# Kernel optimization log

Hardware: AMD Instinct MI355X
Metric: run time of the kernel (lower is better)

The kernel has to match this reference:

```python
import jax, jax.numpy as jnp
import numpy as np

B, G, H, K = 2, 16, 128, 8      # batch, grid side, hidden, edges per grid point
TG = B * G ** 3                  # total grid points = 8192
E = TG * K                       # total edges = 65536
N = 2048                         # total atoms
EPS = 1e-5


def _bn(x, g, b):
    # eval-mode BatchNorm3d with running_mean=0, running_var=1
    s = g / jnp.sqrt(1.0 + EPS)
    return x * s[None, :, None, None, None] + b[None, :, None, None, None]


def _conv(x, w, pad):
    return jax.lax.conv_general_dilated(
        x, w, window_strides=(1, 1, 1), padding=[(pad, pad)] * 3,
        dimension_numbers=("NCDHW", "OIDHW", "NCDHW"))


def _mlp2(x, w1, b1, w2, b2, act):
    return act(x @ w1 + b1) @ w2 + b2


def setup_inputs() -> dict:
    key = jax.random.key(0)
    ks = jax.random.split(key, 16)
    def nrm(k, shape, scale=1.0):
        return jax.random.normal(k, shape, dtype=jnp.float32) * scale
    def lin(k, i, o):
        return nrm(k, (i, o), 1.0 / np.sqrt(i))
    return {
        "node_embedding": nrm(ks[0], (N, H)),
        "node_pos": nrm(ks[1], (N, 3)),
        "grid_pos": nrm(ks[2], (TG, 3)),
        "edge_row": jax.random.randint(ks[3], (E,), 0, N),
        # every grid point covered K times -> bincount never zero (matches original's div-by-bincount)
        "edge_col": jnp.repeat(jnp.arange(TG), K),
        "edge_w1": lin(ks[4], 6, H),    "edge_b1": jnp.zeros(H),
        "edge_w2": lin(ks[5], H, H),    "edge_b2": jnp.zeros(H),
        "msg_w1": lin(ks[6], 2 * H, H), "msg_b1": jnp.zeros(H),
        "msg_w2": lin(ks[7], H, H),     "msg_b2": jnp.zeros(H),
        "upd_w1": lin(ks[8], H, H),     "upd_b1": jnp.zeros(H),
        "upd_w2": lin(ks[9], H, H),     "upd_b2": jnp.zeros(H),
        "in_gamma": jnp.ones(H), "in_beta": jnp.zeros(H),
        "blk_conv1": nrm(ks[10], (3, H, H, 3, 3, 3), 1.0 / np.sqrt(H * 27)),
        "blk_bn1_g": jnp.ones((3, H)), "blk_bn1_b": jnp.zeros((3, H)),
        "blk_conv2": nrm(ks[11], (3, H, H, 3, 3, 3), 1.0 / np.sqrt(H * 27)),
        "blk_bn2_g": jnp.ones((3, H)), "blk_bn2_b": jnp.zeros((3, H)),
        "blk_conv5": nrm(ks[12], (3, H, H, 5, 5, 5), 1.0 / np.sqrt(H * 125)),
        "blk_bns_g": jnp.ones((3, H)), "blk_bns_b": jnp.zeros((3, H)),
        "fc_w": lin(ks[13], H, 20), "fc_b": jnp.zeros(20),
    }


def reference(node_embedding, node_pos, grid_pos, edge_row, edge_col,
              edge_w1, edge_b1, edge_w2, edge_b2,
              msg_w1, msg_b1, msg_w2, msg_b2,
              upd_w1, upd_b1, upd_w2, upd_b2,
              in_gamma, in_beta,
              blk_conv1, blk_bn1_g, blk_bn1_b,
              blk_conv2, blk_bn2_g, blk_bn2_b,
              blk_conv5, blk_bns_g, blk_bns_b,
              fc_w, fc_b):
    silu = jax.nn.silu
    # ---- MPNN message: gather -> edge MLP -> message MLP ----
    edge_attr = jnp.concatenate([node_pos[edge_row], grid_pos[edge_col]], axis=-1)  # [E,6]
    pos_emb = _mlp2(edge_attr, edge_w1, edge_b1, edge_w2, edge_b2, silu)            # [E,H]
    msg_in = jnp.concatenate([node_embedding[edge_row], pos_emb], axis=-1)          # [E,2H]
    message = _mlp2(msg_in, msg_w1, msg_b1, msg_w2, msg_b2, silu)                   # [E,H]
    # ---- scatter-mean onto grid points (global_add_pool / bincount) ----
    agg = jax.ops.segment_sum(message, edge_col, num_segments=TG)
    cnt = jax.ops.segment_sum(jnp.ones((E,), jnp.float32), edge_col, num_segments=TG)
    agg = agg / cnt[:, None]
    x = _mlp2(agg, upd_w1, upd_b1, upd_w2, upd_b2, silu)                            # [TG,H]
    # ---- to dense grid, channels-first ----
    x = x.reshape(B, G, G, G, H).transpose(0, 4, 1, 2, 3)                           # [B,H,G,G,G]
    x = _bn(x, in_gamma, in_beta)
    # ---- 3 residual blocks (eval BN, dropout identity) ----
    for i in range(3):
        left = jax.nn.relu(_bn(_conv(x, blk_conv1[i], 1), blk_bn1_g[i], blk_bn1_b[i]))
        left = _bn(_conv(left, blk_conv2[i], 1), blk_bn2_g[i], blk_bn2_b[i])
        short = _bn(_conv(x, blk_conv5[i], 2), blk_bns_g[i], blk_bns_b[i])
        x = jax.nn.relu(left + short)
    # ---- global max pool (kernel == spatial size) + fc + log_softmax ----
    pooled = x.max(axis=(2, 3, 4))                                                  # [B,H]
    logits = pooled @ fc_w + fc_b                                                   # [B,20]
    return jax.nn.log_softmax(logits, axis=-1)
```

## Files before the change

### kernel.cpp

```cpp
#include <hip/hip_runtime.h>
#include <math.h>


#define EPS_BN 1e-5f

typedef _Float16 f16x8 __attribute__((ext_vector_type(8)));
typedef float f32x4 __attribute__((ext_vector_type(4)));

struct us4 { unsigned short x, y, z, w; };

__device__ __forceinline__ float silu_f(float x) {
  return x / (1.0f + __expf(-x));
}
__device__ __forceinline__ unsigned short f2h(float x) {
  union { _Float16 h; unsigned short u; } v; v.h = (_Float16)x; return v.u;
}
__device__ __forceinline__ float h2f(unsigned short u) {
  union { unsigned short u; _Float16 h; } v; v.u = u; return (float)v.h;
}

template<int AMODE, int KTOT>
__global__ __launch_bounds__(256, 2)
void gemm_k(const float* __restrict__ A,
            const float* __restrict__ W,
            const float* __restrict__ bias,
            const float* __restrict__ pscale,
            const float* __restrict__ pshift,
            float* __restrict__ C,
            int act, int obf)
{
  __shared__ __align__(16) float As[32][68];
  __shared__ __align__(16) float Bs[32][128];
  const int t = threadIdx.x;
  const int mbase = blockIdx.x * 64;
  const int m0 = (t >> 4) << 2;
  const int nA = (t & 15) << 2;
  const int ml = t >> 2;
  const int ks = (t & 3) << 3;

  float acc[4][8];
#pragma unroll
  for (int i = 0; i < 4; i++)
#pragma unroll
    for (int j = 0; j < 8; j++) acc[i][j] = 0.f;

  for (int k0 = 0; k0 < KTOT; k0 += 32) {
    {
      const float* src = A + (size_t)(mbase + ml) * KTOT + (k0 + ks);
      const float4 a0 = *(const float4*)src;
      const float4 a1 = *(const float4*)(src + 4);
      As[ks+0][ml]=a0.x; As[ks+1][ml]=a0.y; As[ks+2][ml]=a0.z; As[ks+3][ml]=a0.w;
      As[ks+4][ml]=a1.x; As[ks+5][ml]=a1.y; As[ks+6][ml]=a1.z; As[ks+7][ml]=a1.w;
    }
    {
      const int kl = t >> 3;
      const int ns = (t & 7) << 4;
      const float* wsrc = W + (size_t)(k0 + kl) * 128 + ns;
      *(float4*)&Bs[kl][ns +  0] = *(const float4*)(wsrc + 0);
      *(float4*)&Bs[kl][ns +  4] = *(const float4*)(wsrc + 4);
      *(float4*)&Bs[kl][ns +  8] = *(const float4*)(wsrc + 8);
      *(float4*)&Bs[kl][ns + 12] = *(const float4*)(wsrc + 12);
    }
    __syncthreads();
#pragma unroll 8
    for (int kk = 0; kk < 32; kk++) {
      const float4 av = *(const float4*)&As[kk][m0];
      const float4 b0 = *(const float4*)&Bs[kk][nA];
      const float4 b1 = *(const float4*)&Bs[kk][nA + 64];
      const float a[4]  = {av.x, av.y, av.z, av.w};
      const float bb[8] = {b0.x, b0.y, b0.z, b0.w, b1.x, b1.y, b1.z, b1.w};
#pragma unroll
      for (int i = 0; i < 4; i++)
#pragma unroll
        for (int j = 0; j < 8; j++)
          acc[i][j] = fmaf(a[i], bb[j], acc[i][j]);
    }
    __syncthreads();
  }

  const float rs = rsqrtf(1.f + EPS_BN);
#pragma unroll
  for (int i = 0; i < 4; i++) {
    const size_t row = (size_t)(mbase + m0 + i);
    float v[8];
#pragma unroll
    for (int j = 0; j < 8; j++) {
      const int col = (j < 4) ? (nA + j) : (nA + 60 + j);
      float x = acc[i][j] + bias[col];
      if (act == 1) x = silu_f(x);
      if (pscale) x = fmaf(x, pscale[col] * rs, pshift[col]);
      v[j] = x;
    }
    if (obf) {
      unsigned short* Cb = (unsigned short*)C;
      us4 r0, r1;
      r0.x=f2h(v[0]); r0.y=f2h(v[1]); r0.z=f2h(v[2]); r0.w=f2h(v[3]);
      r1.x=f2h(v[4]); r1.y=f2h(v[5]); r1.z=f2h(v[6]); r1.w=f2h(v[7]);
      *(us4*)&Cb[row * 128 + nA]      = r0;
      *(us4*)&Cb[row * 128 + nA + 64] = r1;
    } else {
      *(float4*)&C[row * 128 + nA]      = make_float4(v[0], v[1], v[2], v[3]);
      *(float4*)&C[row * 128 + nA + 64] = make_float4(v[4], v[5], v[6], v[7]);
    }
  }
}

__global__ __launch_bounds__(256)
void wpack_g_k(const float* __restrict__ w, unsigned short* __restrict__ wp,
               int total)
{
  const int i = blockIdx.x * 256 + threadIdx.x;
  if (i >= total) return;
  const int j   = i & 7;
  const int l   = (i >> 3) & 63;
  const int nt  = (i >> 9) & 7;
  const int kq  = (i >> 12) & 3;
  const int tap = i >> 14;
  const int k = tap * 128 + kq * 32 + (l >> 4) * 8 + j;
  const int n = nt * 16 + (l & 15);
  wp[i] = f2h(w[(size_t)k * 128 + n]);
}

__global__ __launch_bounds__(256)
void cvt_k(const float* __restrict__ src, unsigned short* __restrict__ dst, int n)
{
  const int i = blockIdx.x * 256 + threadIdx.x;
  if (i < n) dst[i] = f2h(src[i]);
}

template<int AMODE, int TAPS>
__global__ __launch_bounds__(256)
void mgemm_k(const unsigned short* __restrict__ A,
             const unsigned short* __restrict__ emb16,
             const int* __restrict__ rows,
             const int* __restrict__ cols,
             const float* __restrict__ npos,
             const float* __restrict__ gpos,
             const float* __restrict__ ew1,
             const float* __restrict__ eb1,
             const unsigned short* __restrict__ wpanel,
             const float* __restrict__ bias,
             unsigned short* __restrict__ C,
             float* __restrict__ aggout,
             int act)
{
  __shared__ __align__(16) unsigned short Ab[64 * 128];
  __shared__ __align__(16) unsigned short Bb[16384];
  const int t = threadIdx.x;
  const int mbase = blockIdx.x * 64;
  const int l = t & 63, w = t >> 6;
  const int lx = l & 15, lq = l >> 4;
  const int mb = (w >> 1) << 1;
  const int nb = (w & 1) << 2;
  const int rowl = t >> 2;
  const int seg  = t & 3;

  float at0=0,at1=0,at2=0,at3=0,at4=0,at5=0;
  int rowm = 0;
  if (AMODE == 1) {
    const int e = mbase + rowl;
    const int r = rows[e];
    const int g = cols[e];
    at0 = npos[r*3+0]; at1 = npos[r*3+1]; at2 = npos[r*3+2];
    at3 = gpos[g*3+0]; at4 = gpos[g*3+1]; at5 = gpos[g*3+2];
  } else if (AMODE == 2) {
    rowm = rows[mbase + rowl];
  }

  f32x4 acc[2][4];
#pragma unroll
  for (int i = 0; i < 2; i++)
#pragma unroll
    for (int j = 0; j < 4; j++) acc[i][j] = (f32x4){0.f, 0.f, 0.f, 0.f};

  for (int tap = 0; tap < TAPS; tap++) {
    __syncthreads();
    if (AMODE == 1) {
#pragma unroll
      for (int uu = 0; uu < 4; uu++) {
        union { unsigned short h[8]; uint4 v; } pk;
#pragma unroll
        for (int jj = 0; jj < 8; jj++) {
          const int k = seg * 32 + uu * 8 + jj;
          float s = eb1[k];
          s = fmaf(at0, ew1[      k], s);
          s = fmaf(at1, ew1[128 + k], s);
          s = fmaf(at2, ew1[256 + k], s);
          s = fmaf(at3, ew1[384 + k], s);
          s = fmaf(at4, ew1[512 + k], s);
          s = fmaf(at5, ew1[640 + k], s);
          pk.h[jj] = f2h(silu_f(s));
        }
        const int u = seg * 4 + uu;
        *(uint4*)(Ab + (size_t)(rowl * 16 + (u ^ (rowl & 7))) * 8) = pk.v;
      }
    } else {
      const unsigned short* src;
      if (AMODE == 2) {
        src = (tap == 0) ? (emb16 + (size_t)rowm * 128 + seg * 32)
                         : (A + (size_t)(mbase + rowl) * 128 + seg * 32);
      } else {
        src = A + (size_t)(mbase + rowl) * 128 + seg * 32;
      }
#pragma unroll
      for (int uu = 0; uu < 4; uu++) {
        const uint4 v = *(const uint4*)(src + uu * 8);
        const int u = seg * 4 + uu;
        *(uint4*)(Ab + (size_t)(rowl * 16 + (u ^ (rowl & 7))) * 8) = v;
      }
    }
    {
      const unsigned short* g = wpanel + (size_t)tap * 16384 + t * 8;
      unsigned short* dl = Bb + t * 8;
#pragma unroll
      for (int r = 0; r < 8; r++) {
        __builtin_amdgcn_global_load_lds(
            (const __attribute__((address_space(1))) unsigned int*)(g + r * 2048),
            (__attribute__((address_space(3))) unsigned int*)(dl + r * 2048),
            16, 0, 0);
      }
    }
    __syncthreads();
    const int xm = lx & 7;
#pragma unroll
    for (int kq = 0; kq < 4; kq++) {
      f16x8 a0 = *(const f16x8*)(Ab + (size_t)(((mb + 0) * 16 + lx) * 16 + ((kq * 4 + lq) ^ xm)) * 8);
      f16x8 a1 = *(const f16x8*)(Ab + (size_t)(((mb + 1) * 16 + lx) * 16 + ((kq * 4 + lq) ^ xm)) * 8);
      const unsigned short* bbase = Bb + (size_t)((kq * 8 + nb) * 64 + l) * 8;
#pragma unroll
      for (int j = 0; j < 4; j++) {
        f16x8 bv = *(const f16x8*)(bbase + (size_t)j * 512);
        acc[0][j] = __builtin_amdgcn_mfma_f32_16x16x32_f16(a0, bv, acc[0][j], 0, 0, 0);
        acc[1][j] = __builtin_amdgcn_mfma_f32_16x16x32_f16(a1, bv, acc[1][j], 0, 0, 0);
      }
    }
  }

  __syncthreads();
#pragma unroll
  for (int i = 0; i < 2; i++) {
#pragma unroll
    for (int r = 0; r < 4; r++) {
      const int rowloc = (mb + i) * 16 + lq * 4 + r;
#pragma unroll
      for (int j = 0; j < 4; j++) {
        const int col = (nb + j) * 16 + lx;
        float x = acc[i][j][r] + bias[col];
        if (act == 1) x = silu_f(x);
        Ab[rowloc * 128 + col] = f2h(x);
      }
    }
  }
  __syncthreads();
  if (aggout) {
#pragma unroll
    for (int q = t * 4; q < t * 4 + 4; q++) {
      const int g = q >> 7, c = q & 127;
      float s = 0.f;
#pragma unroll
      for (int r = 0; r < 8; r++) s += h2f(Ab[(g * 8 + r) * 128 + c]);
      aggout[(size_t)((mbase >> 3) + g) * 128 + c] = s * 0.125f;
    }
  } else {
    const size_t base = (size_t)(mbase + rowl) * 128 + seg * 32;
#pragma unroll
    for (int uu = 0; uu < 4; uu++)
      *(uint4*)(C + base + uu * 8) = *(const uint4*)(Ab + rowl * 128 + seg * 32 + uu * 8);
  }
}

__global__ __launch_bounds__(256)
void wpack_k(const float* __restrict__ w, unsigned short* __restrict__ wp, int T)
{
  const int i = blockIdx.x * 256 + threadIdx.x;
  if (i >= 3 * 4 * 8 * 64 * 8) return;
  const int j  = i & 7;
  const int l  = (i >> 3) & 63;
  const int nt = (i >> 9) & 7;
  const int kq = (i >> 12) & 3;
  const int ib = i >> 14;
  const int o = nt * 16 + (l & 15);
  const int c = kq * 32 + (l >> 4) * 8 + j;
  const float* src = w + ((size_t)(ib * 128 + o) * 128 + c) * T;
  unsigned short* dst = wp + (size_t)(ib * T) * 16384
                           + (size_t)(kq * 8 + nt) * 512 + l * 8 + j;
  for (int tp = 0; tp < T; tp++)
    dst[(size_t)tp * 16384] = f2h(src[tp]);
}

template<int KS>
__global__ __launch_bounds__(256, 1)
void convmf_k(const unsigned short* __restrict__ xin,
              const unsigned short* __restrict__ wpack,
              float* __restrict__ part)
{
  constexpr int P  = KS / 2;
  constexpr int SW = 16 + 2 * P;
  __shared__ __align__(16) unsigned short Ab[4 * SW * 128];
  __shared__ __align__(16) unsigned short Bb[16384];

  const int t   = threadIdx.x;
  const int bx  = blockIdx.x;
  const int kd  = bx >> 7;
  const int rem = bx & 127;
  const int b   = rem >> 6;
  const int z   = (rem >> 2) & 15;
  const int y0  = (rem & 3) << 2;
  const int zz  = z + kd - P;
  float* pout = part + (size_t)kd * (8192 * 128);
  const size_t obase = ((size_t)((b * 16 + z) * 16 + y0) * 16) * 128;

  if ((unsigned)zz >= 16u) {
    float4 zf = make_float4(0, 0, 0, 0);
    float4* dst = (float4*)(pout + obase);
    for (int i = t; i < 2048; i += 256) dst[i] = zf;
    return;
  }

  const int l  = t & 63, w = t >> 6;
  const int lx = l & 15, lq = l >> 4;
  const int mb = (w >> 1) << 1;
  const int nb = (w & 1) << 2;

  f32x4 acc[2][4];
#pragma unroll
  for (int i = 0; i < 2; i++)
#pragma unroll
    for (int j = 0; j < 4; j++) acc[i][j] = (f32x4){0.f, 0.f, 0.f, 0.f};

  const unsigned short* inplane = xin + ((size_t)(b * 16 + zz) * 256) * 128;
  const unsigned short* wkd = wpack + (size_t)(kd * KS * KS) * 16384;

  for (int kh = 0; kh < KS; kh++) {
    __syncthreads();
    for (int idx = t; idx < 4 * SW * 16; idx += 256) {
      const int ry = idx / (SW * 16);
      const int r2 = idx - ry * (SW * 16);
      const int xs = r2 >> 4;
      const int u  = r2 & 15;
      const int y  = y0 + ry + kh - P;
      const int x  = xs - P;
      uint4 val = make_uint4(0, 0, 0, 0);
      if ((unsigned)y < 16u && (unsigned)x < 16u)
        val = *(const uint4*)(inplane + ((size_t)(y * 16 + x)) * 128 + u * 8);
      const int du = (ry * SW + xs) * 16 + (u ^ (xs & 7));
      *(uint4*)(Ab + (size_t)du * 8) = val;
    }
    const unsigned short* wkh = wkd + (size_t)(kh * KS) * 16384;
    for (int kw = 0; kw < KS; kw++) {
      __syncthreads();
      {
        const unsigned short* g = wkh + (size_t)kw * 16384 + t * 8;
        unsigned short* dl = Bb + t * 8;
#pragma unroll
        for (int r = 0; r < 8; r++) {
          __builtin_amdgcn_global_load_lds(
              (const __attribute__((address_space(1))) unsigned int*)(g + r * 2048),
              (__attribute__((address_space(3))) unsigned int*)(dl + r * 2048),
              16, 0, 0);
        }
      }
      __syncthreads();
      const int xsw = lx + kw;
      const int xm  = xsw & 7;
#pragma unroll
      for (int kq = 0; kq < 4; kq++) {
        f16x8 a0 = *(const f16x8*)(Ab + (size_t)(((mb + 0) * SW + xsw) * 16 + ((kq * 4 + lq) ^ xm)) * 8);
        f16x8 a1 = *(const f16x8*)(Ab + (size_t)(((mb + 1) * SW + xsw) * 16 + ((kq * 4 + lq) ^ xm)) * 8);
        const unsigned short* bbase = Bb + (size_t)((kq * 8 + nb) * 64 + l) * 8;
#pragma unroll
        for (int j = 0; j < 4; j++) {
          f16x8 bv = *(const f16x8*)(bbase + (size_t)j * 512);
          acc[0][j] = __builtin_amdgcn_mfma_f32_16x16x32_f16(a0, bv, acc[0][j], 0, 0, 0);
          acc[1][j] = __builtin_amdgcn_mfma_f32_16x16x32_f16(a1, bv, acc[1][j], 0, 0, 0);
        }
      }
    }
  }

#pragma unroll
  for (int i = 0; i < 2; i++) {
    const int my = mb + i;
#pragma unroll
    for (int r = 0; r < 4; r++) {
      const size_t vrow = obase + (size_t)(my * 16 + lq * 4 + r) * 128;
#pragma unroll
      for (int j = 0; j < 4; j++)
        pout[vrow + (nb + j) * 16 + lx] = acc[i][j][r];
    }
  }
}

__global__ __launch_bounds__(256)
void combine1_k(const float* __restrict__ p,
                const float* __restrict__ g, const float* __restrict__ be,
                unsigned short* __restrict__ o)
{
  const int i = blockIdx.x * 256 + threadIdx.x;
  const size_t off = (size_t)i * 4;
  const int c = (i & 31) * 4;
  float4 a0 = *(const float4*)(p + off);
  float4 a1 = *(const float4*)(p + 1048576 + off);
  float4 a2 = *(const float4*)(p + 2097152 + off);
  const float rs = rsqrtf(1.f + EPS_BN);
  float4 gg = *(const float4*)(g + c);
  float4 bb = *(const float4*)(be + c);
  float v0 = fmaxf(fmaf(a0.x + a1.x + a2.x, gg.x * rs, bb.x), 0.f);
  float v1 = fmaxf(fmaf(a0.y + a1.y + a2.y, gg.y * rs, bb.y), 0.f);
  float v2 = fmaxf(fmaf(a0.z + a1.z + a2.z, gg.z * rs, bb.z), 0.f);
  float v3 = fmaxf(fmaf(a0.w + a1.w + a2.w, gg.w * rs, bb.w), 0.f);
  us4 r; r.x = f2h(v0); r.y = f2h(v1); r.z = f2h(v2); r.w = f2h(v3);
  *(us4*)(o + off) = r;
}

__global__ __launch_bounds__(256)
void combine2_k(const float* __restrict__ p2, const float* __restrict__ p5,
                const float* __restrict__ g2, const float* __restrict__ b2,
                const float* __restrict__ gs, const float* __restrict__ bs,
                unsigned short* __restrict__ o)
{
  const int i = blockIdx.x * 256 + threadIdx.x;
  const size_t off = (size_t)i * 4;
  const int c = (i & 31) * 4;
  float4 s2 = *(const float4*)(p2 + off);
  {
    float4 a1 = *(const float4*)(p2 + 1048576 + off);
    float4 a2 = *(const float4*)(p2 + 2097152 + off);
    s2.x += a1.x + a2.x; s2.y += a1.y + a2.y;
    s2.z += a1.z + a2.z; s2.w += a1.w + a2.w;
  }
  float4 s5 = *(const float4*)(p5 + off);
#pragma unroll
  for (int gi = 1; gi < 5; gi++) {
    float4 a = *(const float4*)(p5 + (size_t)gi * 1048576 + off);
    s5.x += a.x; s5.y += a.y; s5.z += a.z; s5.w += a.w;
  }
  const float rs = rsqrtf(1.f + EPS_BN);
  float4 gg2 = *(const float4*)(g2 + c);
  float4 bb2 = *(const float4*)(b2 + c);
  float4 ggs = *(const float4*)(gs + c);
  float4 bbs = *(const float4*)(bs + c);
  float v0 = fmaxf(fmaf(s2.x, gg2.x * rs, bb2.x) + fmaf(s5.x, ggs.x * rs, bbs.x), 0.f);
  float v1 = fmaxf(fmaf(s2.y, gg2.y * rs, bb2.y) + fmaf(s5.y, ggs.y * rs, bbs.y), 0.f);
  float v2 = fmaxf(fmaf(s2.z, gg2.z * rs, bb2.z) + fmaf(s5.z, ggs.z * rs, bbs.z), 0.f);
  float v3 = fmaxf(fmaf(s2.w, gg2.w * rs, bb2.w) + fmaf(s5.w, ggs.w * rs, bbs.w), 0.f);
  us4 r; r.x = f2h(v0); r.y = f2h(v1); r.z = f2h(v2); r.w = f2h(v3);
  *(us4*)(o + off) = r;
}

__global__ __launch_bounds__(256)
void pool_partial_k(const unsigned short* __restrict__ xg, float* __restrict__ pmax)
{
  __shared__ float red[256];
  const int bz = blockIdx.x;
  const int t = threadIdx.x;
  const int c = t & 127;
  const int h = t >> 7;
  const unsigned short* base = xg + (size_t)bz * 256 * 128;
  float m = -3.4e38f;
  for (int i = 0; i < 128; i++)
    m = fmaxf(m, h2f(base[(size_t)(h * 128 + i) * 128 + c]));
  red[t] = m;
  __syncthreads();
  if (t < 128) pmax[bz * 128 + t] = fmaxf(red[t], red[t + 128]);
}

__global__ __launch_bounds__(256)
void final_k(const float* __restrict__ pmax,
             const float* __restrict__ fc_w,
             const float* __restrict__ fc_b,
             float* __restrict__ outp)
{
  __shared__ float pool[2][128];
  __shared__ float lg[2][20];
  const int t = threadIdx.x;
  const int b = t >> 7;
  const int c = t & 127;
  float m = -3.4e38f;
  for (int zi = 0; zi < 16; zi++)
    m = fmaxf(m, pmax[(b * 16 + zi) * 128 + c]);
  pool[b][c] = m;
  __syncthreads();
  if (t < 40) {
    const int bb = t / 20, j = t % 20;
    float l = fc_b[j];
    for (int cc = 0; cc < 128; cc++)
      l = fmaf(pool[bb][cc], fc_w[cc * 20 + j], l);
    lg[bb][j] = l;
  }
  __syncthreads();
  if (t < 2) {
    float mx = -3.4e38f;
    for (int j = 0; j < 20; j++) mx = fmaxf(mx, lg[t][j]);
    float s = 0.f;
    for (int j = 0; j < 20; j++) s += expf(lg[t][j] - mx);
    const float ls = mx + logf(s);
    for (int j = 0; j < 20; j++) outp[t * 20 + j] = lg[t][j] - ls;
  }
}

extern "C" void kernel_launch(void* const* d_in, const int* in_sizes, int n_in,
                              void* d_out, int out_size, void* d_ws, size_t ws_size,
                              hipStream_t stream) {
  (void)in_sizes; (void)n_in; (void)out_size; (void)ws_size;
  const float* node_embedding = (const float*)d_in[0];
  const float* node_pos  = (const float*)d_in[1];
  const float* grid_pos  = (const float*)d_in[2];
  const int*   edge_row  = (const int*)d_in[3];
  const int*   edge_col  = (const int*)d_in[4];
  const float* edge_w1   = (const float*)d_in[5];
  const float* edge_b1   = (const float*)d_in[6];
  const float* edge_w2   = (const float*)d_in[7];
  const float* edge_b2   = (const float*)d_in[8];
  const float* msg_w1    = (const float*)d_in[9];
  const float* msg_b1    = (const float*)d_in[10];
  const float* msg_w2    = (const float*)d_in[11];
  const float* msg_b2    = (const float*)d_in[12];
  const float* upd_w1    = (const float*)d_in[13];
  const float* upd_b1    = (const float*)d_in[14];
  const float* upd_w2    = (const float*)d_in[15];
  const float* upd_b2    = (const float*)d_in[16];
  const float* in_gamma  = (const float*)d_in[17];
  const float* in_beta   = (const float*)d_in[18];
  const float* blk_conv1 = (const float*)d_in[19];
  const float* blk_bn1_g = (const float*)d_in[20];
  const float* blk_bn1_b = (const float*)d_in[21];
  const float* blk_conv2 = (const float*)d_in[22];
  const float* blk_bn2_g = (const float*)d_in[23];
  const float* blk_bn2_b = (const float*)d_in[24];
  const float* blk_conv5 = (const float*)d_in[25];
  const float* blk_bns_g = (const float*)d_in[26];
  const float* blk_bns_b = (const float*)d_in[27];
  const float* fc_w      = (const float*)d_in[28];
  const float* fc_b      = (const float*)d_in[29];

  float* ws = (float*)d_ws;
  unsigned short* bufA = (unsigned short*)ws;
  unsigned short* bufB = (unsigned short*)(ws + 4194304);
  unsigned short* wp31 = (unsigned short*)ws;
  unsigned short* wp32 = (unsigned short*)(ws + 663552);
  unsigned short* wp5  = (unsigned short*)(ws + 1327104);
  float* p1   = ws + 4400128;
  float* p2   = ws + 7545856;
  float* p5   = ws + 10691584;
  unsigned short* xg0 = (unsigned short*)(ws + 16000000);
  unsigned short* xg1 = (unsigned short*)(ws + 16524288);
  unsigned short* tg  = (unsigned short*)(ws + 17048576);
  float* agg  = ws + 17572864;
  float* u1   = ws + 18621440;
  float* pmax = ws + 19670016;
  unsigned short* emb16 = (unsigned short*)(ws + 19675136);
  unsigned short* wg_e2 = (unsigned short*)(ws + 19806208);
  unsigned short* wg_m1 = (unsigned short*)(ws + 19814400);
  unsigned short* wg_m2 = (unsigned short*)(ws + 19830784);
  float* outF = (float*)d_out;

  cvt_k<<<1024, 256, 0, stream>>>(node_embedding, emb16, 2048 * 128);
  wpack_g_k<<<64, 256, 0, stream>>>(edge_w2, wg_e2, 16384);
  wpack_g_k<<<128, 256, 0, stream>>>(msg_w1, wg_m1, 32768);
  wpack_g_k<<<64, 256, 0, stream>>>(msg_w2, wg_m2, 16384);

  mgemm_k<1, 1><<<1024, 256, 0, stream>>>(
      nullptr, nullptr, edge_row, edge_col, node_pos, grid_pos, edge_w1, edge_b1,
      wg_e2, edge_b2, bufA, nullptr, 0);
  mgemm_k<2, 2><<<1024, 256, 0, stream>>>(
      bufA, emb16, edge_row, nullptr, nullptr, nullptr, nullptr, nullptr,
      wg_m1, msg_b1, bufB, nullptr, 1);
  mgemm_k<0, 1><<<1024, 256, 0, stream>>>(
      bufB, nullptr, nullptr, nullptr, nullptr, nullptr, nullptr, nullptr,
      wg_m2, msg_b2, bufB, agg, 0);

  wpack_k<<<192, 256, 0, stream>>>(blk_conv1, wp31, 27);
  wpack_k<<<192, 256, 0, stream>>>(blk_conv2, wp32, 27);
  wpack_k<<<192, 256, 0, stream>>>(blk_conv5, wp5, 125);

  gemm_k<0, 128><<<128, 256, 0, stream>>>(
      agg, upd_w1, upd_b1, nullptr, nullptr, u1, 1, 0);
  gemm_k<0, 128><<<128, 256, 0, stream>>>(
      u1, upd_w2, upd_b2, in_gamma, in_beta, (float*)xg0, 0, 1);

  const unsigned short* xin = xg0;
  unsigned short* xout = xg1;
  for (int i = 0; i < 3; i++) {
    convmf_k<3><<<384, 256, 0, stream>>>(xin, wp31 + (size_t)i * 27 * 16384, p1);
    combine1_k<<<1024, 256, 0, stream>>>(p1, blk_bn1_g + i * 128, blk_bn1_b + i * 128, tg);
    convmf_k<3><<<384, 256, 0, stream>>>(tg, wp32 + (size_t)i * 27 * 16384, p2);
    convmf_k<5><<<640, 256, 0, stream>>>(xin, wp5 + (size_t)i * 125 * 16384, p5);
    combine2_k<<<1024, 256, 0, stream>>>(p2, p5,
        blk_bn2_g + i * 128, blk_bn2_b + i * 128,
        blk_bns_g + i * 128, blk_bns_b + i * 128, xout);
    unsigned short* tmp = (unsigned short*)xin;
    xin = xout;
    xout = tmp;
  }

  pool_partial_k<<<32, 256, 0, stream>>>(xin, pmax);
  final_k<<<1, 256, 0, stream>>>(pmax, fc_w, fc_b, outF);
}
```

Baseline: 558.8 us.

## Fuse edge and message MLP GEMMs into one per-tile kernel; parallelize conv weight packing

Replaces the three edge/message GEMM launches with one kernel that keeps each 64-edge tile's intermediates in shared memory across all four weight panels, then writes the per-grid-point mean. This removes the global round trips for the edge and message hidden buffers and two launches. The last layer's output is also reduced in fp32 instead of fp16. Separately, conv weight packing now uses one thread per packed element instead of a serial loop over taps, giving far more parallelism. The fused kernel uses more shared memory and launch_bounds(256,1), which may lower occupancy.

Result: faster. 525.8 us (-5.9%).

```diff
diff --git a/kernel.cpp b/kernel.cpp
--- a/kernel.cpp
+++ b/kernel.cpp
@@ -128,24 +128,83 @@
   if (i < n) dst[i] = f2h(src[i]);
 }
 
-template<int AMODE, int TAPS>
-__global__ __launch_bounds__(256)
-void mgemm_k(const unsigned short* __restrict__ A,
-             const unsigned short* __restrict__ emb16,
-             const int* __restrict__ rows,
-             const int* __restrict__ cols,
-             const float* __restrict__ npos,
-             const float* __restrict__ gpos,
-             const float* __restrict__ ew1,
-             const float* __restrict__ eb1,
-             const unsigned short* __restrict__ wpanel,
-             const float* __restrict__ bias,
-             unsigned short* __restrict__ C,
-             float* __restrict__ aggout,
-             int act)
-{
-  __shared__ __align__(16) unsigned short Ab[64 * 128];
+__device__ __forceinline__ void stage_b(const unsigned short* g,
+                                        unsigned short* dl) {
+#pragma unroll
+  for (int r = 0; r < 8; r++)
+    __builtin_amdgcn_global_load_lds(
+        (const __attribute__((address_space(1))) unsigned int*)(g + r * 2048),
+        (__attribute__((address_space(3))) unsigned int*)(dl + r * 2048),
+        16, 0, 0);
+}
+
+__device__ __forceinline__ void mfma_tile(const unsigned short* Aswz,
+                                          const unsigned short* Bb,
+                                          int mb, int nb, int lx, int lq, int l,
+                                          f32x4 acc[2][4]) {
+  const int xm = lx & 7;
+#pragma unroll
+  for (int kq = 0; kq < 4; kq++) {
+    f16x8 a0 = *(const f16x8*)(Aswz + (size_t)(((mb + 0) * 16 + lx) * 16 + ((kq * 4 + lq) ^ xm)) * 8);
+    f16x8 a1 = *(const f16x8*)(Aswz + (size_t)(((mb + 1) * 16 + lx) * 16 + ((kq * 4 + lq) ^ xm)) * 8);
+    const unsigned short* bbase = Bb + (size_t)((kq * 8 + nb) * 64 + l) * 8;
+#pragma unroll
+    for (int j = 0; j < 4; j++) {
+      f16x8 bv = *(const f16x8*)(bbase + (size_t)j * 512);
+      acc[0][j] = __builtin_amdgcn_mfma_f32_16x16x32_f16(a0, bv, acc[0][j], 0, 0, 0);
+      acc[1][j] = __builtin_amdgcn_mfma_f32_16x16x32_f16(a1, bv, acc[1][j], 0, 0, 0);
+    }
+  }
+}
+
+__device__ __forceinline__ void epi_h(const f32x4 acc[2][4],
+                                      const float* bias, int act,
+                                      unsigned short* dst,
+                                      int mb, int nb, int lx, int lq) {
+#pragma unroll
+  for (int i = 0; i < 2; i++)
+#pragma unroll
+    for (int r = 0; r < 4; r++) {
+      const int rowloc = (mb + i) * 16 + lq * 4 + r;
+#pragma unroll
+      for (int j = 0; j < 4; j++) {
+        const int col = (nb + j) * 16 + lx;
+        float x = acc[i][j][r] + bias[col];
+        if (act) x = silu_f(x);
+        dst[rowloc * 128 + col] = f2h(x);
+      }
+    }
+}
+
+__device__ __forceinline__ void restage(const unsigned short* src,
+                                        unsigned short* Aswz,
+                                        int rowl, int seg) {
+#pragma unroll
+  for (int uu = 0; uu < 4; uu++) {
+    uint4 v = *(const uint4*)(src + rowl * 128 + seg * 32 + uu * 8);
+    const int u = seg * 4 + uu;
+    *(uint4*)(Aswz + (size_t)(rowl * 16 + (u ^ (rowl & 7))) * 8) = v;
+  }
+}
+
+__global__ __launch_bounds__(256, 1)
+void mpnn_k(const unsigned short* __restrict__ emb16,
+            const int* __restrict__ rows,
+            const int* __restrict__ cols,
+            const float* __restrict__ npos,
+            const float* __restrict__ gpos,
+            const float* __restrict__ ew1,
+            const float* __restrict__ eb1,
+            const float* __restrict__ eb2,
+            const float* __restrict__ mb1,
+            const float* __restrict__ mb2,
+            const unsigned short* __restrict__ wall,
+            float* __restrict__ aggout)
+{
+  __shared__ __align__(16) unsigned short Aswz[8192];
+  __shared__ __align__(16) unsigned short Cpl[8192];
   __shared__ __align__(16) unsigned short Bb[16384];
+
   const int t = threadIdx.x;
   const int mbase = blockIdx.x * 64;
   const int l = t & 63, w = t >> 6;
@@ -155,137 +214,125 @@
   const int rowl = t >> 2;
   const int seg  = t & 3;
 
-  float at0=0,at1=0,at2=0,at3=0,at4=0,at5=0;
-  int rowm = 0;
-  if (AMODE == 1) {
-    const int e = mbase + rowl;
-    const int r = rows[e];
-    const int g = cols[e];
-    at0 = npos[r*3+0]; at1 = npos[r*3+1]; at2 = npos[r*3+2];
-    at3 = gpos[g*3+0]; at4 = gpos[g*3+1]; at5 = gpos[g*3+2];
-  } else if (AMODE == 2) {
-    rowm = rows[mbase + rowl];
-  }
-
-  f32x4 acc[2][4];
+  const int e = mbase + rowl;
+  const int rr = rows[e];
+  const int gg = cols[e];
+  const float at0 = npos[rr*3+0], at1 = npos[rr*3+1], at2 = npos[rr*3+2];
+  const float at3 = gpos[gg*3+0], at4 = gpos[gg*3+1], at5 = gpos[gg*3+2];
+
+#pragma unroll
+  for (int uu = 0; uu < 4; uu++) {
+    union { unsigned short h[8]; uint4 v; } pk;
+#pragma unroll
+    for (int jj = 0; jj < 8; jj++) {
+      const int k = seg * 32 + uu * 8 + jj;
+      float s = eb1[k];
+      s = fmaf(at0, ew1[      k], s);
+      s = fmaf(at1, ew1[128 + k], s);
+      s = fmaf(at2, ew1[256 + k], s);
+      s = fmaf(at3, ew1[384 + k], s);
+      s = fmaf(at4, ew1[512 + k], s);
+      s = fmaf(at5, ew1[640 + k], s);
+      pk.h[jj] = f2h(silu_f(s));
+    }
+    const int u = seg * 4 + uu;
+    *(uint4*)(Aswz + (size_t)(rowl * 16 + (u ^ (rowl & 7))) * 8) = pk.v;
+  }
+  stage_b(wall + t * 8, Bb + t * 8);
+  __syncthreads();
+
+  f32x4 acc1[2][4];
 #pragma unroll
   for (int i = 0; i < 2; i++)
 #pragma unroll
-    for (int j = 0; j < 4; j++) acc[i][j] = (f32x4){0.f, 0.f, 0.f, 0.f};
-
-  for (int tap = 0; tap < TAPS; tap++) {
-    __syncthreads();
-    if (AMODE == 1) {
-#pragma unroll
-      for (int uu = 0; uu < 4; uu++) {
-        union { unsigned short h[8]; uint4 v; } pk;
-#pragma unroll
-        for (int jj = 0; jj < 8; jj++) {
-          const int k = seg * 32 + uu * 8 + jj;
-          float s = eb1[k];
-          s = fmaf(at0, ew1[      k], s);
-          s = fmaf(at1, ew1[128 + k], s);
-          s = fmaf(at2, ew1[256 + k], s);
-          s = fmaf(at3, ew1[384 + k], s);
-          s = fmaf(at4, ew1[512 + k], s);
-          s = fmaf(at5, ew1[640 + k], s);
-          pk.h[jj] = f2h(silu_f(s));
-        }
-        const int u = seg * 4 + uu;
-        *(uint4*)(Ab + (size_t)(rowl * 16 + (u ^ (rowl & 7))) * 8) = pk.v;
-      }
-    } else {
-      const unsigned short* src;
-      if (AMODE == 2) {
-        src = (tap == 0) ? (emb16 + (size_t)rowm * 128 + seg * 32)
-                         : (A + (size_t)(mbase + rowl) * 128 + seg * 32);
-      } else {
-        src = A + (size_t)(mbase + rowl) * 128 + seg * 32;
-      }
-#pragma unroll
-      for (int uu = 0; uu < 4; uu++) {
-        const uint4 v = *(const uint4*)(src + uu * 8);
-        const int u = seg * 4 + uu;
-        *(uint4*)(Ab + (size_t)(rowl * 16 + (u ^ (rowl & 7))) * 8) = v;
-      }
-    }
-    {
-      const unsigned short* g = wpanel + (size_t)tap * 16384 + t * 8;
-      unsigned short* dl = Bb + t * 8;
-#pragma unroll
-      for (int r = 0; r < 8; r++) {
-        __builtin_amdgcn_global_load_lds(
-            (const __attribute__((address_space(1))) unsigned int*)(g + r * 2048),
-            (__attribute__((address_space(3))) unsigned int*)(dl + r * 2048),
-            16, 0, 0);
-      }
-    }
-    __syncthreads();
-    const int xm = lx & 7;
-#pragma unroll
-    for (int kq = 0; kq < 4; kq++) {
-      f16x8 a0 = *(const f16x8*)(Ab + (size_t)(((mb + 0) * 16 + lx) * 16 + ((kq * 4 + lq) ^ xm)) * 8);
-      f16x8 a1 = *(const f16x8*)(Ab + (size_t)(((mb + 1) * 16 + lx) * 16 + ((kq * 4 + lq) ^ xm)) * 8);
-      const unsigned short* bbase = Bb + (size_t)((kq * 8 + nb) * 64 + l) * 8;
-#pragma unroll
-      for (int j = 0; j < 4; j++) {
-        f16x8 bv = *(const f16x8*)(bbase + (size_t)j * 512);
-        acc[0][j] = __builtin_amdgcn_mfma_f32_16x16x32_f16(a0, bv, acc[0][j], 0, 0, 0);
-        acc[1][j] = __builtin_amdgcn_mfma_f32_16x16x32_f16(a1, bv, acc[1][j], 0, 0, 0);
-      }
-    }
-  }
-
-  __syncthreads();
-#pragma unroll
-  for (int i = 0; i < 2; i++) {
+    for (int j = 0; j < 4; j++) acc1[i][j] = (f32x4){0.f,0.f,0.f,0.f};
+  mfma_tile(Aswz, Bb, mb, nb, lx, lq, l, acc1);
+  __syncthreads();
+
+  epi_h(acc1, eb2, 0, Cpl, mb, nb, lx, lq);
+  {
+    const unsigned short* src = emb16 + (size_t)rr * 128 + seg * 32;
+#pragma unroll
+    for (int uu = 0; uu < 4; uu++) {
+      const uint4 v = *(const uint4*)(src + uu * 8);
+      const int u = seg * 4 + uu;
+      *(uint4*)(Aswz + (size_t)(rowl * 16 + (u ^ (rowl & 7))) * 8) = v;
+    }
+  }
+  stage_b(wall + 16384 + t * 8, Bb + t * 8);
+  __syncthreads();
+
+  f32x4 acc2[2][4];
+#pragma unroll
+  for (int i = 0; i < 2; i++)
+#pragma unroll
+    for (int j = 0; j < 4; j++) acc2[i][j] = (f32x4){0.f,0.f,0.f,0.f};
+  mfma_tile(Aswz, Bb, mb, nb, lx, lq, l, acc2);
+  __syncthreads();
+
+  stage_b(wall + 32768 + t * 8, Bb + t * 8);
+  restage(Cpl, Aswz, rowl, seg);
+  __syncthreads();
+
+  mfma_tile(Aswz, Bb, mb, nb, lx, lq, l, acc2);
+  __syncthreads();
+
+  epi_h(acc2, mb1, 1, Cpl, mb, nb, lx, lq);
+  stage_b(wall + 49152 + t * 8, Bb + t * 8);
+  __syncthreads();
+
+  restage(Cpl, Aswz, rowl, seg);
+  __syncthreads();
+
+  f32x4 acc3[2][4];
+#pragma unroll
+  for (int i = 0; i < 2; i++)
+#pragma unroll
+    for (int j = 0; j < 4; j++) acc3[i][j] = (f32x4){0.f,0.f,0.f,0.f};
+  mfma_tile(Aswz, Bb, mb, nb, lx, lq, l, acc3);
+  __syncthreads();
+
+  float* Bf = (float*)Bb;
+#pragma unroll
+  for (int i = 0; i < 2; i++)
 #pragma unroll
     for (int r = 0; r < 4; r++) {
       const int rowloc = (mb + i) * 16 + lq * 4 + r;
 #pragma unroll
       for (int j = 0; j < 4; j++) {
         const int col = (nb + j) * 16 + lx;
-        float x = acc[i][j][r] + bias[col];
-        if (act == 1) x = silu_f(x);
-        Ab[rowloc * 128 + col] = f2h(x);
+        Bf[rowloc * 128 + col] = acc3[i][j][r] + mb2[col];
       }
     }
-  }
-  __syncthreads();
-  if (aggout) {
-#pragma unroll
-    for (int q = t * 4; q < t * 4 + 4; q++) {
-      const int g = q >> 7, c = q & 127;
-      float s = 0.f;
-#pragma unroll
-      for (int r = 0; r < 8; r++) s += h2f(Ab[(g * 8 + r) * 128 + c]);
-      aggout[(size_t)((mbase >> 3) + g) * 128 + c] = s * 0.125f;
-    }
-  } else {
-    const size_t base = (size_t)(mbase + rowl) * 128 + seg * 32;
-#pragma unroll
-    for (int uu = 0; uu < 4; uu++)
-      *(uint4*)(C + base + uu * 8) = *(const uint4*)(Ab + rowl * 128 + seg * 32 + uu * 8);
+  __syncthreads();
+
+#pragma unroll
+  for (int qq = 0; qq < 4; qq++) {
+    const int q = t * 4 + qq;
+    const int g = q >> 7, c = q & 127;
+    float s = 0.f;
+#pragma unroll
+    for (int r = 0; r < 8; r++) s += Bf[(g * 8 + r) * 128 + c];
+    aggout[(size_t)((mbase >> 3) + g) * 128 + c] = s * 0.125f;
   }
 }
 
 __global__ __launch_bounds__(256)
-void wpack_k(const float* __restrict__ w, unsigned short* __restrict__ wp, int T)
+void wpack_k(const float* __restrict__ w, unsigned short* __restrict__ wp,
+             int T, int total)
 {
   const int i = blockIdx.x * 256 + threadIdx.x;
-  if (i >= 3 * 4 * 8 * 64 * 8) return;
+  if (i >= total) return;
   const int j  = i & 7;
   const int l  = (i >> 3) & 63;
   const int nt = (i >> 9) & 7;
   const int kq = (i >> 12) & 3;
-  const int ib = i >> 14;
+  const int r  = i >> 14;
+  const int tap = r % T;
+  const int ib  = r / T;
   const int o = nt * 16 + (l & 15);
   const int c = kq * 32 + (l >> 4) * 8 + j;
-  const float* src = w + ((size_t)(ib * 128 + o) * 128 + c) * T;
-  unsigned short* dst = wp + (size_t)(ib * T) * 16384
-                           + (size_t)(kq * 8 + nt) * 512 + l * 8 + j;
-  for (int tp = 0; tp < T; tp++)
-    dst[(size_t)tp * 16384] = f2h(src[tp]);
+  wp[i] = f2h(w[((size_t)(ib * 128 + o) * 128 + c) * T + tap]);
 }
 
 template<int KS>
@@ -349,17 +396,7 @@
     const unsigned short* wkh = wkd + (size_t)(kh * KS) * 16384;
     for (int kw = 0; kw < KS; kw++) {
       __syncthreads();
-      {
-        const unsigned short* g = wkh + (size_t)kw * 16384 + t * 8;
-        unsigned short* dl = Bb + t * 8;
-#pragma unroll
-        for (int r = 0; r < 8; r++) {
-          __builtin_amdgcn_global_load_lds(
-              (const __attribute__((address_space(1))) unsigned int*)(g + r * 2048),
-              (__attribute__((address_space(3))) unsigned int*)(dl + r * 2048),
-              16, 0, 0);
-        }
-      }
+      stage_b(wkh + (size_t)kw * 16384 + t * 8, Bb + t * 8);
       __syncthreads();
       const int xsw = lx + kw;
       const int xm  = xsw & 7;
@@ -535,8 +572,6 @@
   const float* fc_b      = (const float*)d_in[29];
 
   float* ws = (float*)d_ws;
-  unsigned short* bufA = (unsigned short*)ws;
-  unsigned short* bufB = (unsigned short*)(ws + 4194304);
   unsigned short* wp31 = (unsigned short*)ws;
   unsigned short* wp32 = (unsigned short*)(ws + 663552);
   unsigned short* wp5  = (unsigned short*)(ws + 1327104);
@@ -549,30 +584,21 @@
   float* agg  = ws + 17572864;
   float* u1   = ws + 18621440;
   float* pmax = ws + 19670016;
-  unsigned short* emb16 = (unsigned short*)(ws + 19675136);
-  unsigned short* wg_e2 = (unsigned short*)(ws + 19806208);
-  unsigned short* wg_m1 = (unsigned short*)(ws + 19814400);
-  unsigned short* wg_m2 = (unsigned short*)(ws + 19830784);
+  unsigned short* emb16  = (unsigned short*)(ws + 19675136);
+  unsigned short* wg_all = (unsigned short*)(ws + 19806208);
   float* outF = (float*)d_out;
 
   cvt_k<<<1024, 256, 0, stream>>>(node_embedding, emb16, 2048 * 128);
-  wpack_g_k<<<64, 256, 0, stream>>>(edge_w2, wg_e2, 16384);
-  wpack_g_k<<<128, 256, 0, stream>>>(msg_w1, wg_m1, 32768);
-  wpack_g_k<<<64, 256, 0, stream>>>(msg_w2, wg_m2, 16384);
-
-  mgemm_k<1, 1><<<1024, 256, 0, stream>>>(
-      nullptr, nullptr, edge_row, edge_col, node_pos, grid_pos, edge_w1, edge_b1,
-      wg_e2, edge_b2, bufA, nullptr, 0);
-  mgemm_k<2, 2><<<1024, 256, 0, stream>>>(
-      bufA, emb16, edge_row, nullptr, nullptr, nullptr, nullptr, nullptr,
-      wg_m1, msg_b1, bufB, nullptr, 1);
-  mgemm_k<0, 1><<<1024, 256, 0, stream>>>(
-      bufB, nullptr, nullptr, nullptr, nullptr, nullptr, nullptr, nullptr,
-      wg_m2, msg_b2, bufB, agg, 0);
-
-  wpack_k<<<192, 256, 0, stream>>>(blk_conv1, wp31, 27);
-  wpack_k<<<192, 256, 0, stream>>>(blk_conv2, wp32, 27);
-  wpack_k<<<192, 256, 0, stream>>>(blk_conv5, wp5, 125);
+  wpack_g_k<<<64, 256, 0, stream>>>(edge_w2, wg_all, 16384);
+  wpack_g_k<<<128, 256, 0, stream>>>(msg_w1, wg_all + 16384, 32768);
+  wpack_g_k<<<64, 256, 0, stream>>>(msg_w2, wg_all + 49152, 16384);
+  wpack_k<<<5184, 256, 0, stream>>>(blk_conv1, wp31, 27, 3 * 27 * 16384);
+  wpack_k<<<5184, 256, 0, stream>>>(blk_conv2, wp32, 27, 3 * 27 * 16384);
+  wpack_k<<<24000, 256, 0, stream>>>(blk_conv5, wp5, 125, 3 * 125 * 16384);
+
+  mpnn_k<<<1024, 256, 0, stream>>>(
+      emb16, edge_row, edge_col, node_pos, grid_pos, edge_w1, edge_b1,
+      edge_b2, msg_b1, msg_b2, wg_all, agg);
 
   gemm_k<0, 128><<<128, 256, 0, stream>>>(
       agg, upd_w1, upd_b1, nullptr, nullptr, u1, 1, 0);
```
